# Kernel tuning notes

Measured on AMD Instinct MI355X. Metric: run time of the kernel, lower is better.

Reference implementation:

```python
import jax, jax.numpy as jnp
import numpy as np

B, T, D, H, L, O = 128, 512, 256, 1024, 2, 1


def _cell(x, h, s, Wax, Uas, ba, Wih, Whh, bh):
    # alpha-t gate, exponential smoothing of hidden state, then candidate
    alpha = jax.nn.sigmoid(x @ Wax.T + s @ Uas.T + ba)        # [B,H]
    s_new = alpha * h + (1.0 - alpha) * s                      # smoothed hidden
    h_new = jnp.tanh(x @ Wih.T + s_new @ Whh.T + bh)           # new hidden
    return h_new, s_new


def setup_inputs() -> dict:
    key = jax.random.key(0)
    ks = jax.random.split(key, 12)
    sd_in = 1.0 / np.sqrt(D)
    sd_h = 1.0 / np.sqrt(H)
    return {
        "input": jax.random.normal(ks[0], (B, T, D), dtype=jnp.float32),
        "Wax0": jax.random.normal(ks[1], (H, D), dtype=jnp.float32) * sd_in,
        "Uas0": jax.random.normal(ks[2], (H, H), dtype=jnp.float32) * sd_h,
        "ba0": jnp.zeros((H,), jnp.float32),
        "Wih0": jax.random.normal(ks[3], (H, D), dtype=jnp.float32) * sd_in,
        "Whh0": jax.random.normal(ks[4], (H, H), dtype=jnp.float32) * sd_h,
        "bh0": jnp.zeros((H,), jnp.float32),
        "Wax1": jax.random.normal(ks[5], (H, H), dtype=jnp.float32) * sd_h,
        "Uas1": jax.random.normal(ks[6], (H, H), dtype=jnp.float32) * sd_h,
        "ba1": jnp.zeros((H,), jnp.float32),
        "Wih1": jax.random.normal(ks[7], (H, H), dtype=jnp.float32) * sd_h,
        "Whh1": jax.random.normal(ks[8], (H, H), dtype=jnp.float32) * sd_h,
        "bh1": jnp.zeros((H,), jnp.float32),
        "fc_W": jax.random.normal(ks[9], (O, H), dtype=jnp.float32) * sd_h,
        "fc_b": jnp.zeros((O,), jnp.float32),
    }


def reference(input, Wax0, Uas0, ba0, Wih0, Whh0, bh0,
              Wax1, Uas1, ba1, Wih1, Whh1, bh1, fc_W, fc_b):
    b = input.shape[0]
    zeros = jnp.zeros((b, H), input.dtype)
    carry0 = (zeros, zeros, zeros, zeros)  # h0, s0, h1, s1

    def step(carry, x_t):
        h0, s0, h1, s1 = carry
        h0, s0 = _cell(x_t, h0, s0, Wax0, Uas0, ba0, Wih0, Whh0, bh0)
        h1, s1 = _cell(h0, h1, s1, Wax1, Uas1, ba1, Wih1, Whh1, bh1)
        return (h0, s0, h1, s1), None

    xs = jnp.transpose(input, (1, 0, 2))  # [T,B,D]
    (h0, s0, h1, s1), _ = jax.lax.scan(step, carry0, xs)
    out = h1 @ fc_W.T + fc_b  # [B,O]
    hidden = jnp.stack([h0, h1])          # [L,B,H]
    smoothed = jnp.stack([s0, s1])        # [L,B,H]
    return (out, hidden, smoothed)
```

## Files before the change

kernel.cpp:

```cpp
#include <hip/hip_runtime.h>


typedef unsigned short u16;
typedef unsigned long long u64;
typedef __attribute__((ext_vector_type(8))) short short8;
typedef __attribute__((ext_vector_type(4))) float f32x4;

#define NB   128
#define TT   512
#define DD   256
#define HH   1024
#define NTHR 512
#define SPAN (NB * HH)
#define RING 32
#define GS   16

#define S0_OFF  0u
#define S1_OFF  524288u
#define H0_OFF  1048576u
#define FL_OFF  9437184u
#define W_OFF   9486336u
#define NBIG    6291456u

__device__ __forceinline__ u16 f2bf(float f) {
    unsigned u = __builtin_bit_cast(unsigned, f);
    return (u16)((u + 0x7fffu + ((u >> 16) & 1u)) >> 16);
}
__device__ __forceinline__ u64 agent_load64(const u64* p) {
    return __hip_atomic_load(p, __ATOMIC_RELAXED, __HIP_MEMORY_SCOPE_AGENT);
}
__device__ __forceinline__ void agent_store64(u64* p, u64 v) {
    __hip_atomic_store(p, v, __ATOMIC_RELAXED, __HIP_MEMORY_SCOPE_AGENT);
}

__device__ __forceinline__ void flag_set(unsigned* f, int wgl, unsigned val, int tid)
{
    __syncthreads();
    if (tid == 0)
        __hip_atomic_store(f + wgl * 16, val, __ATOMIC_RELEASE,
                           __HIP_MEMORY_SCOPE_AGENT);
}
__device__ __forceinline__ void flag_wait(unsigned* f, unsigned val, int tid)
{
    if (tid < GS)
        while (__hip_atomic_load(f + tid * 16, __ATOMIC_RELAXED,
                                 __HIP_MEMORY_SCOPE_AGENT) < val)
            __builtin_amdgcn_s_sleep(1);
    __syncthreads();
}

__device__ __forceinline__ void load_frags(short8* fr, const u16* base,
                                           int row, int wv, int lkg)
{
    const u16* sp = base + ((size_t)row << 10) + wv * 128 + lkg * 8;
    #pragma unroll
    for (int s = 0; s < 4; ++s) {
        union { short8 v; u64 q[2]; } u_;
        u_.q[0] = agent_load64((const u64*)(sp + s * 32));
        u_.q[1] = agent_load64((const u64*)(sp + s * 32 + 4));
        fr[s] = u_.v;
    }
}

__device__ __forceinline__ void mm4(f32x4* a, const short8* fr, const u16* W,
                                    int n0, int lrow, int wv, int lkg)
{
    #pragma unroll
    for (int nt = 0; nt < 4; ++nt) {
        const u16* wp = W + ((size_t)(n0 + nt * 16 + lrow) << 10) + wv * 128 + lkg * 8;
        #pragma unroll
        for (int s = 0; s < 4; ++s)
            a[nt] = __builtin_amdgcn_mfma_f32_16x16x32_bf16(
                *(const short8*)(wp + s * 32), fr[s], a[nt], 0, 0, 0);
    }
}

__device__ __forceinline__ void mmx4(f32x4* a, const float* xrow, const u16* W,
                                     int n0, int lrow, int wv, int lkg)
{
    const float* p = xrow + wv * 32 + lkg * 8;
    float4 A = *(const float4*)p;
    float4 B = *(const float4*)(p + 4);
    short8 v;
    v[0]=(short)f2bf(A.x); v[1]=(short)f2bf(A.y); v[2]=(short)f2bf(A.z); v[3]=(short)f2bf(A.w);
    v[4]=(short)f2bf(B.x); v[5]=(short)f2bf(B.y); v[6]=(short)f2bf(B.z); v[7]=(short)f2bf(B.w);
    #pragma unroll
    for (int nt = 0; nt < 4; ++nt) {
        const u16* wp = W + ((size_t)(n0 + nt * 16 + lrow) << 8) + wv * 32 + lkg * 8;
        a[nt] = __builtin_amdgcn_mfma_f32_16x16x32_bf16(
            *(const short8*)wp, v, a[nt], 0, 0, 0);
    }
}

__device__ __forceinline__ void red_put(float (*red)[4][8][64], const f32x4* a,
                                        int wv, int lane)
{
    #pragma unroll
    for (int nt = 0; nt < 4; ++nt)
        #pragma unroll
        for (int c = 0; c < 4; ++c) red[c][nt][wv][lane] = a[nt][c];
}
__device__ __forceinline__ f32x4 red_get(float (*red)[4][8][64], int nt, int lane)
{
    f32x4 v = {0.f, 0.f, 0.f, 0.f};
    #pragma unroll
    for (int j = 0; j < 8; ++j)
        #pragma unroll
        for (int c = 0; c < 4; ++c) v[c] += red[c][nt][j][lane];
    return v;
}

__device__ __forceinline__ u64 pack4(float a, float b, float c, float d)
{
    return (u64)f2bf(a) | ((u64)f2bf(b) << 16) | ((u64)f2bf(c) << 32)
         | ((u64)f2bf(d) << 48);
}

__global__ void conv_weights(const float* Uas0, const float* Whh0, const float* Wax1,
                             const float* Uas1, const float* Wih1, const float* Whh1,
                             const float* Wax0, const float* Wih0, u16* dst)
{
    for (size_t i = (size_t)blockIdx.x * blockDim.x + threadIdx.x; i < 6815744u;
         i += (size_t)gridDim.x * blockDim.x) {
        const float* src; size_t off;
        if (i < NBIG) {
            int seg = (int)(i >> 20); off = i & 1048575u;
            src = seg == 0 ? Uas0 : seg == 1 ? Whh0 : seg == 2 ? Wax1
                : seg == 3 ? Uas1 : seg == 4 ? Wih1 : Whh1;
        } else {
            size_t j = i - NBIG; off = j & 262143u;
            src = (j >> 18) ? Wih0 : Wax0;
        }
        dst[i] = f2bf(src[off]);
    }
}

extern "C" __global__ void __launch_bounds__(NTHR, 1)
alphat_mfma(const float* __restrict__ x,
            const u16* __restrict__ wUas0, const u16* __restrict__ wWhh0,
            const u16* __restrict__ wWax1, const u16* __restrict__ wUas1,
            const u16* __restrict__ wWih1, const u16* __restrict__ wWhh1,
            const u16* __restrict__ wWax0, const u16* __restrict__ wWih0,
            const float* __restrict__ ba0, const float* __restrict__ bh0,
            const float* __restrict__ ba1, const float* __restrict__ bh1,
            const float* __restrict__ fcW, const float* __restrict__ fcb,
            float* __restrict__ out,
            u16* s0b, u16* s1b, u16* h0r, unsigned* flags)
{
    __shared__ float red[4][4][8][64];

    const int tid  = threadIdx.x;
    const int wv   = tid >> 6;
    const int lane = tid & 63;
    const int lrow = lane & 15;
    const int lkg  = lane >> 4;

    const bool isL0 = (blockIdx.x < 128);
    const int wg  = isL0 ? blockIdx.x : (blockIdx.x - 128);
    const int ngg = (wg & 7) * 2 + ((wg >> 3) & 1);
    const int mg  = wg >> 4;
    const int wgl = wg & 15;
    const int m0  = mg * 16;
    const int n0  = ngg * 64;

    unsigned* fB = flags + (size_t)mg * 256;
    unsigned* fC = flags + 2048 + (size_t)mg * 256;
    unsigned* fD = flags + 4096 + (size_t)mg * 256;

    const int arow = m0 + lrow;
    const bool own = (wv < 4);
    const int nb   = n0 + (wv & 3) * 16 + lkg * 4;

    const f32x4 zf = {0.f, 0.f, 0.f, 0.f};
    const size_t HIDB = NB, SMOB = NB + 2 * (size_t)SPAN;

    if (isL0) {
        float4 vba0 = {0,0,0,0}, vbh0 = {0,0,0,0};
        if (own) { vba0 = *(const float4*)(ba0 + nb); vbh0 = *(const float4*)(bh0 + nb); }
        float h0l[4] = {0,0,0,0}, s0l[4] = {0,0,0,0};

        short8 frags[4];
        #pragma unroll
        for (int s = 0; s < 4; ++s)
            #pragma unroll
            for (int i = 0; i < 8; ++i) frags[s][i] = 0;
        const float* xbase = x + (size_t)arow * (TT * DD);
        f32x4 pBx[4], pAx[4];
        #pragma unroll
        for (int nt = 0; nt < 4; ++nt) { pBx[nt] = zf; pAx[nt] = zf; }
        mmx4(pBx, xbase + 0 * DD, wWih0, n0, lrow, wv, lkg);
        mmx4(pAx, xbase + 1 * DD, wWax0, n0, lrow, wv, lkg);

        for (int t = 0; t < TT; ++t) {
            u16* h0cur = h0r + (size_t)(t & (RING - 1)) * SPAN;
            u16* s0nxt = s0b + ((t + 1) & 1) * SPAN;

            if (t >= RING) flag_wait(fC, (unsigned)(t - RING + 1), tid);

            f32x4 acc[4], pA[4];
            #pragma unroll
            for (int nt = 0; nt < 4; ++nt) { acc[nt] = pBx[nt]; pA[nt] = pAx[nt]; }
            mm4(acc, frags, wWhh0, n0, lrow, wv, lkg);
            mm4(pA,  frags, wUas0, n0, lrow, wv, lkg);

            red_put(red, acc, wv, lane);
            __syncthreads();
            f32x4 hsum = zf;
            if (own) hsum = red_get(red, wv, lane);
            __syncthreads();
            red_put(red, pA, wv, lane);
            __syncthreads();
            if (own) {
                f32x4 asum = red_get(red, wv, lane);
                float hb[4];
                #pragma unroll
                for (int r = 0; r < 4; ++r) {
                    hb[r] = tanhf(hsum[r] + ((const float*)&vbh0)[r]);
                    h0l[r] = hb[r];
                }
                agent_store64((u64*)(h0cur + (size_t)(m0 + lrow) * HH + nb),
                              pack4(hb[0], hb[1], hb[2], hb[3]));
                if (t + 1 < TT) {
                    float sb[4];
                    #pragma unroll
                    for (int r = 0; r < 4; ++r) {
                        float al = 1.f / (1.f + __expf(-(asum[r] + ((const float*)&vba0)[r])));
                        sb[r] = al * hb[r] + (1.f - al) * s0l[r];
                        s0l[r] = sb[r];
                    }
                    agent_store64((u64*)(s0nxt + (size_t)(m0 + lrow) * HH + nb),
                                  pack4(sb[0], sb[1], sb[2], sb[3]));
                }
            }
            flag_set(fB, wgl, (unsigned)(t + 1), tid);

            if (t + 1 < TT) {
                #pragma unroll
                for (int nt = 0; nt < 4; ++nt) pBx[nt] = zf;
                mmx4(pBx, xbase + (size_t)(t + 1) * DD, wWih0, n0, lrow, wv, lkg);
                if (t + 2 < TT) {
                    #pragma unroll
                    for (int nt = 0; nt < 4; ++nt) pAx[nt] = zf;
                    mmx4(pAx, xbase + (size_t)(t + 2) * DD, wWax0, n0, lrow, wv, lkg);
                }
                flag_wait(fB, (unsigned)(t + 1), tid);
                load_frags(frags, s0nxt, arow, wv, lkg);
            }
        }
        if (own) {
            const size_t o = (size_t)(m0 + lrow) * HH + nb;
            *(float4*)(out + HIDB + o) = make_float4(h0l[0], h0l[1], h0l[2], h0l[3]);
            *(float4*)(out + SMOB + o) = make_float4(s0l[0], s0l[1], s0l[2], s0l[3]);
        }
    } else {
        float4 vba1 = {0,0,0,0}, vbh1 = {0,0,0,0};
        if (own) { vba1 = *(const float4*)(ba1 + nb); vbh1 = *(const float4*)(bh1 + nb); }
        float h1l[4] = {0,0,0,0}, s1l[4] = {0,0,0,0};
        f32x4 pC1[4];
        #pragma unroll
        for (int nt = 0; nt < 4; ++nt) pC1[nt] = zf;

        for (int t = 0; t < TT; ++t) {
            u16* h0cur = h0r + (size_t)(t & (RING - 1)) * SPAN;
            u16* s1cur = s1b + (t & 1) * SPAN;

            if (t >= 2) flag_wait(fD, (unsigned)(t - 1), tid);

            flag_wait(fB, (unsigned)(t + 1), tid);
            short8 fh[4];
            load_frags(fh, h0cur, arow, wv, lkg);

            f32x4 c[4];
            #pragma unroll
            for (int nt = 0; nt < 4; ++nt) c[nt] = pC1[nt];
            mm4(c, fh, wWax1, n0, lrow, wv, lkg);
            red_put(red, c, wv, lane);
            __syncthreads();
            if (own) {
                f32x4 csum = red_get(red, wv, lane);
                float sb[4];
                #pragma unroll
                for (int r = 0; r < 4; ++r) {
                    float al = 1.f / (1.f + __expf(-(csum[r] + ((const float*)&vba1)[r])));
                    sb[r] = al * h1l[r] + (1.f - al) * s1l[r];
                    s1l[r] = sb[r];
                }
                agent_store64((u64*)(s1cur + (size_t)(m0 + lrow) * HH + nb),
                              pack4(sb[0], sb[1], sb[2], sb[3]));
            }
            flag_set(fC, wgl, (unsigned)(t + 1), tid);

            f32x4 pD1[4];
            #pragma unroll
            for (int nt = 0; nt < 4; ++nt) pD1[nt] = zf;
            mm4(pD1, fh, wWih1, n0, lrow, wv, lkg);

            flag_wait(fC, (unsigned)(t + 1), tid);
            short8 fs1[4];
            load_frags(fs1, s1cur, arow, wv, lkg);
            mm4(pD1, fs1, wWhh1, n0, lrow, wv, lkg);
            #pragma unroll
            for (int nt = 0; nt < 4; ++nt) pC1[nt] = zf;
            mm4(pC1, fs1, wUas1, n0, lrow, wv, lkg);
            red_put(red, pD1, wv, lane);
            __syncthreads();
            if (own) {
                f32x4 dsum = red_get(red, wv, lane);
                #pragma unroll
                for (int r = 0; r < 4; ++r)
                    h1l[r] = tanhf(dsum[r] + ((const float*)&vbh1)[r]);
            }
            flag_set(fD, wgl, (unsigned)(t + 1), tid);
        }
        if (own) {
            const size_t o = (size_t)(m0 + lrow) * HH + nb;
            *(float4*)(out + HIDB + SPAN + o) = make_float4(h1l[0], h1l[1], h1l[2], h1l[3]);
            *(float4*)(out + SMOB + SPAN + o) = make_float4(s1l[0], s1l[1], s1l[2], s1l[3]);

            const float4 w4 = *(const float4*)(fcW + nb);
            float v = h1l[0] * w4.x + h1l[1] * w4.y + h1l[2] * w4.z + h1l[3] * w4.w;
            v += __shfl_xor(v, 16);
            v += __shfl_xor(v, 32);
            if (lane < 16) {
                if (ngg == 0 && wv == 0) v += fcb[0];
                atomicAdd(out + m0 + lane, v);
            }
        }
    }
}

extern "C" void kernel_launch(void* const* d_in, const int* in_sizes, int n_in,
                              void* d_out, int out_size, void* d_ws, size_t ws_size,
                              hipStream_t stream)
{
    const float* x    = (const float*)d_in[0];
    const float* Wax0 = (const float*)d_in[1];
    const float* Uas0 = (const float*)d_in[2];
    const float* ba0  = (const float*)d_in[3];
    const float* Wih0 = (const float*)d_in[4];
    const float* Whh0 = (const float*)d_in[5];
    const float* bh0  = (const float*)d_in[6];
    const float* Wax1 = (const float*)d_in[7];
    const float* Uas1 = (const float*)d_in[8];
    const float* ba1  = (const float*)d_in[9];
    const float* Wih1 = (const float*)d_in[10];
    const float* Whh1 = (const float*)d_in[11];
    const float* bh1  = (const float*)d_in[12];
    const float* fcW  = (const float*)d_in[13];
    const float* fcb  = (const float*)d_in[14];
    float* out = (float*)d_out;

    char* ws = (char*)d_ws;
    u16* s0b = (u16*)(ws + S0_OFF);
    u16* s1b = (u16*)(ws + S1_OFF);
    u16* h0r = (u16*)(ws + H0_OFF);
    unsigned* flags = (unsigned*)(ws + FL_OFF);
    u16* wbase = (u16*)(ws + W_OFF);
    u16* wUas0 = wbase + 0 * 1048576;
    u16* wWhh0 = wbase + 1 * 1048576;
    u16* wWax1 = wbase + 2 * 1048576;
    u16* wUas1 = wbase + 3 * 1048576;
    u16* wWih1 = wbase + 4 * 1048576;
    u16* wWhh1 = wbase + 5 * 1048576;
    u16* wWax0 = wbase + 6 * 1048576;
    u16* wWih0 = wbase + 6 * 1048576 + 262144;

    hipMemsetAsync(d_ws, 0, W_OFF, stream);
    hipMemsetAsync(d_out, 0, (size_t)out_size * sizeof(float), stream);

    conv_weights<<<dim3(1024), dim3(256), 0, stream>>>(
        Uas0, Whh0, Wax1, Uas1, Wih1, Whh1, Wax0, Wih0, wbase);

    alphat_mfma<<<dim3(256), dim3(NTHR), 0, stream>>>(
        x, wUas0, wWhh0, wWax1, wUas1, wWih1, wWhh1, wWax0, wWih0,
        ba0, bh0, ba1, bh1, fcW, fcb, out, s0b, s1b, h0r, flags);
}
```

Baseline: 10.33 ms.

## Replace block-wide flag barriers with per-wave waits and merge reductions

```diff
diff --git a/kernel.cpp b/kernel.cpp
--- a/kernel.cpp
+++ b/kernel.cpp
@@ -35,18 +35,28 @@
 
 __device__ __forceinline__ void flag_set(unsigned* f, int wgl, unsigned val, int tid)
 {
-    __syncthreads();
     if (tid == 0)
         __hip_atomic_store(f + wgl * 16, val, __ATOMIC_RELEASE,
                            __HIP_MEMORY_SCOPE_AGENT);
 }
-__device__ __forceinline__ void flag_wait(unsigned* f, unsigned val, int tid)
-{
-    if (tid < GS)
-        while (__hip_atomic_load(f + tid * 16, __ATOMIC_RELAXED,
+__device__ __forceinline__ void wait2(unsigned* f, int wv, unsigned val, int lane)
+{
+    if (lane < 2) {
+        const int p = lane ? (wv + 8) : wv;
+        while (__hip_atomic_load(f + p * 16, __ATOMIC_RELAXED,
                                  __HIP_MEMORY_SCOPE_AGENT) < val)
             __builtin_amdgcn_s_sleep(1);
-    __syncthreads();
+    }
+    asm volatile("" ::: "memory");
+}
+__device__ __forceinline__ void wait_all(unsigned* f, unsigned val, int lane)
+{
+    if (lane < GS) {
+        while (__hip_atomic_load(f + lane * 16, __ATOMIC_RELAXED,
+                                 __HIP_MEMORY_SCOPE_AGENT) < val)
+            __builtin_amdgcn_s_sleep(1);
+    }
+    asm volatile("" ::: "memory");
 }
 
 __device__ __forceinline__ void load_frags(short8* fr, const u16* base,
@@ -92,22 +102,26 @@
     }
 }
 
-__device__ __forceinline__ void red_put(float (*red)[4][8][64], const f32x4* a,
-                                        int wv, int lane)
+__device__ __forceinline__ void red_put(float (*red)[4][4][7][64], int q,
+                                        const f32x4* a, int wv, int lane)
 {
     #pragma unroll
-    for (int nt = 0; nt < 4; ++nt)
+    for (int nt = 0; nt < 4; ++nt) {
+        if (nt != wv) {
+            const int j = (wv < nt) ? wv : wv - 1;
+            #pragma unroll
+            for (int c = 0; c < 4; ++c) red[q][c][nt][j][lane] = a[nt][c];
+        }
+    }
+}
+__device__ __forceinline__ f32x4 red_get(float (*red)[4][4][7][64], int q,
+                                         f32x4 own, int nt, int lane)
+{
+    #pragma unroll
+    for (int j = 0; j < 7; ++j)
         #pragma unroll
-        for (int c = 0; c < 4; ++c) red[c][nt][wv][lane] = a[nt][c];
-}
-__device__ __forceinline__ f32x4 red_get(float (*red)[4][8][64], int nt, int lane)
-{
-    f32x4 v = {0.f, 0.f, 0.f, 0.f};
-    #pragma unroll
-    for (int j = 0; j < 8; ++j)
-        #pragma unroll
-        for (int c = 0; c < 4; ++c) v[c] += red[c][nt][j][lane];
-    return v;
+        for (int c = 0; c < 4; ++c) own[c] += red[q][c][nt][j][lane];
+    return own;
 }
 
 __device__ __forceinline__ u64 pack4(float a, float b, float c, float d)
@@ -147,7 +161,7 @@
             float* __restrict__ out,
             u16* s0b, u16* s1b, u16* h0r, unsigned* flags)
 {
-    __shared__ float red[4][4][8][64];
+    __shared__ float red[2][4][4][7][64];
 
     const int tid  = threadIdx.x;
     const int wv   = tid >> 6;
@@ -195,7 +209,10 @@
             u16* h0cur = h0r + (size_t)(t & (RING - 1)) * SPAN;
             u16* s0nxt = s0b + ((t + 1) & 1) * SPAN;
 
-            if (t >= RING) flag_wait(fC, (unsigned)(t - RING + 1), tid);
+            if (own) {
+                wait_all(fB, (unsigned)t, lane);
+                if (t >= RING) wait_all(fC, (unsigned)(t - RING + 1), lane);
+            }
 
             f32x4 acc[4], pA[4];
             #pragma unroll
@@ -203,15 +220,16 @@
             mm4(acc, frags, wWhh0, n0, lrow, wv, lkg);
             mm4(pA,  frags, wUas0, n0, lrow, wv, lkg);
 
-            red_put(red, acc, wv, lane);
-            __syncthreads();
-            f32x4 hsum = zf;
-            if (own) hsum = red_get(red, wv, lane);
-            __syncthreads();
-            red_put(red, pA, wv, lane);
+            red_put(red, 0, acc, wv, lane);
+            red_put(red, 1, pA,  wv, lane);
             __syncthreads();
             if (own) {
-                f32x4 asum = red_get(red, wv, lane);
+                f32x4 accOwn = zf, pAOwn = zf;
+                #pragma unroll
+                for (int nt = 0; nt < 4; ++nt)
+                    if (nt == wv) { accOwn = acc[nt]; pAOwn = pA[nt]; }
+                f32x4 hsum = red_get(red, 0, accOwn, wv, lane);
+                f32x4 asum = red_get(red, 1, pAOwn,  wv, lane);
                 float hb[4];
                 #pragma unroll
                 for (int r = 0; r < 4; ++r) {
@@ -232,6 +250,7 @@
                                   pack4(sb[0], sb[1], sb[2], sb[3]));
                 }
             }
+            __syncthreads();
             flag_set(fB, wgl, (unsigned)(t + 1), tid);
 
             if (t + 1 < TT) {
@@ -243,7 +262,7 @@
                     for (int nt = 0; nt < 4; ++nt) pAx[nt] = zf;
                     mmx4(pAx, xbase + (size_t)(t + 2) * DD, wWax0, n0, lrow, wv, lkg);
                 }
-                flag_wait(fB, (unsigned)(t + 1), tid);
+                wait2(fB, wv, (unsigned)(t + 1), lane);
                 load_frags(frags, s0nxt, arow, wv, lkg);
             }
         }
@@ -259,25 +278,34 @@
         f32x4 pC1[4];
         #pragma unroll
         for (int nt = 0; nt < 4; ++nt) pC1[nt] = zf;
+        f32x4 dOwn = zf;
+
+        short8 fh[4];
+        wait2(fB, wv, 1u, lane);
+        load_frags(fh, h0r, arow, wv, lkg);
 
         for (int t = 0; t < TT; ++t) {
-            u16* h0cur = h0r + (size_t)(t & (RING - 1)) * SPAN;
             u16* s1cur = s1b + (t & 1) * SPAN;
 
-            if (t >= 2) flag_wait(fD, (unsigned)(t - 1), tid);
-
-            flag_wait(fB, (unsigned)(t + 1), tid);
-            short8 fh[4];
-            load_frags(fh, h0cur, arow, wv, lkg);
+            if (own && t >= 2) wait_all(fD, (unsigned)(t - 1), lane);
 
             f32x4 c[4];
             #pragma unroll
             for (int nt = 0; nt < 4; ++nt) c[nt] = pC1[nt];
             mm4(c, fh, wWax1, n0, lrow, wv, lkg);
-            red_put(red, c, wv, lane);
+            red_put(red, 0, c, wv, lane);
             __syncthreads();
             if (own) {
-                f32x4 csum = red_get(red, wv, lane);
+                if (t > 0) {
+                    f32x4 dsum = red_get(red, 1, dOwn, wv, lane);
+                    #pragma unroll
+                    for (int r = 0; r < 4; ++r)
+                        h1l[r] = tanhf(dsum[r] + ((const float*)&vbh1)[r]);
+                }
+                f32x4 cOwn = zf;
+                #pragma unroll
+                for (int nt = 0; nt < 4; ++nt) if (nt == wv) cOwn = c[nt];
+                f32x4 csum = red_get(red, 0, cOwn, wv, lane);
                 float sb[4];
                 #pragma unroll
                 for (int r = 0; r < 4; ++r) {
@@ -288,31 +316,39 @@
                 agent_store64((u64*)(s1cur + (size_t)(m0 + lrow) * HH + nb),
                               pack4(sb[0], sb[1], sb[2], sb[3]));
             }
+            __syncthreads();
             flag_set(fC, wgl, (unsigned)(t + 1), tid);
 
             f32x4 pD1[4];
             #pragma unroll
             for (int nt = 0; nt < 4; ++nt) pD1[nt] = zf;
             mm4(pD1, fh, wWih1, n0, lrow, wv, lkg);
-
-            flag_wait(fC, (unsigned)(t + 1), tid);
+            if (t + 1 < TT) {
+                wait2(fB, wv, (unsigned)(t + 2), lane);
+                load_frags(fh, h0r + (size_t)((t + 1) & (RING - 1)) * SPAN,
+                           arow, wv, lkg);
+            }
+
+            wait2(fC, wv, (unsigned)(t + 1), lane);
             short8 fs1[4];
             load_frags(fs1, s1cur, arow, wv, lkg);
             mm4(pD1, fs1, wWhh1, n0, lrow, wv, lkg);
             #pragma unroll
             for (int nt = 0; nt < 4; ++nt) pC1[nt] = zf;
             mm4(pC1, fs1, wUas1, n0, lrow, wv, lkg);
-            red_put(red, pD1, wv, lane);
+            red_put(red, 1, pD1, wv, lane);
+            #pragma unroll
+            for (int nt = 0; nt < 4; ++nt) if (nt == wv) dOwn = pD1[nt];
             __syncthreads();
-            if (own) {
-                f32x4 dsum = red_get(red, wv, lane);
-                #pragma unroll
-                for (int r = 0; r < 4; ++r)
-                    h1l[r] = tanhf(dsum[r] + ((const float*)&vbh1)[r]);
-            }
             flag_set(fD, wgl, (unsigned)(t + 1), tid);
         }
+
         if (own) {
+            f32x4 dsum = red_get(red, 1, dOwn, wv, lane);
+            #pragma unroll
+            for (int r = 0; r < 4; ++r)
+                h1l[r] = tanhf(dsum[r] + ((const float*)&vbh1)[r]);
+
             const size_t o = (size_t)(m0 + lrow) * HH + nb;
             *(float4*)(out + HIDB + SPAN + o) = make_float4(h1l[0], h1l[1], h1l[2], h1l[3]);
             *(float4*)(out + SMOB + SPAN + o) = make_float4(s1l[0], s1l[1], s1l[2], s1l[3]);
```

Measured after the change: 11.80 ms. 14.2% more time.

## Keep recurrent weight tiles in registers and prefetch next-step layer-1 input GEMM

Applied to the files above, without the earlier changes.

```diff
diff --git a/kernel.cpp b/kernel.cpp
--- a/kernel.cpp
+++ b/kernel.cpp
@@ -60,6 +60,27 @@
         u_.q[1] = agent_load64((const u64*)(sp + s * 32 + 4));
         fr[s] = u_.v;
     }
+}
+
+__device__ __forceinline__ void load_wreg(short8* w, const u16* W,
+                                          int n0, int lrow, int wv, int lkg)
+{
+    #pragma unroll
+    for (int nt = 0; nt < 4; ++nt)
+        #pragma unroll
+        for (int s = 0; s < 4; ++s)
+            w[nt * 4 + s] = *(const short8*)(W
+                + ((size_t)(n0 + nt * 16 + lrow) << 10) + wv * 128 + s * 32 + lkg * 8);
+}
+
+__device__ __forceinline__ void mm4r(f32x4* a, const short8* fr, const short8* w)
+{
+    #pragma unroll
+    for (int nt = 0; nt < 4; ++nt)
+        #pragma unroll
+        for (int s = 0; s < 4; ++s)
+            a[nt] = __builtin_amdgcn_mfma_f32_16x16x32_bf16(
+                w[nt * 4 + s], fr[s], a[nt], 0, 0, 0);
 }
 
 __device__ __forceinline__ void mm4(f32x4* a, const short8* fr, const u16* W,
@@ -175,6 +196,10 @@
     const size_t HIDB = NB, SMOB = NB + 2 * (size_t)SPAN;
 
     if (isL0) {
+        short8 wh[16], wu[16];
+        load_wreg(wh, wWhh0, n0, lrow, wv, lkg);
+        load_wreg(wu, wUas0, n0, lrow, wv, lkg);
+
         float4 vba0 = {0,0,0,0}, vbh0 = {0,0,0,0};
         if (own) { vba0 = *(const float4*)(ba0 + nb); vbh0 = *(const float4*)(bh0 + nb); }
         float h0l[4] = {0,0,0,0}, s0l[4] = {0,0,0,0};
@@ -200,8 +225,8 @@
             f32x4 acc[4], pA[4];
             #pragma unroll
             for (int nt = 0; nt < 4; ++nt) { acc[nt] = pBx[nt]; pA[nt] = pAx[nt]; }
-            mm4(acc, frags, wWhh0, n0, lrow, wv, lkg);
-            mm4(pA,  frags, wUas0, n0, lrow, wv, lkg);
+            mm4r(acc, frags, wh);
+            mm4r(pA,  frags, wu);
 
             red_put(red, acc, wv, lane);
             __syncthreads();
@@ -253,27 +278,32 @@
             *(float4*)(out + SMOB + o) = make_float4(s0l[0], s0l[1], s0l[2], s0l[3]);
         }
     } else {
+        short8 wu1[16], wh1[16];
+        load_wreg(wu1, wUas1, n0, lrow, wv, lkg);
+        load_wreg(wh1, wWhh1, n0, lrow, wv, lkg);
+
         float4 vba1 = {0,0,0,0}, vbh1 = {0,0,0,0};
         if (own) { vba1 = *(const float4*)(ba1 + nb); vbh1 = *(const float4*)(bh1 + nb); }
         float h1l[4] = {0,0,0,0}, s1l[4] = {0,0,0,0};
-        f32x4 pC1[4];
+        f32x4 pC1[4], cAx[4];
         #pragma unroll
         for (int nt = 0; nt < 4; ++nt) pC1[nt] = zf;
 
+        short8 fh[4];
+        flag_wait(fB, 1u, tid);
+        load_frags(fh, h0r, arow, wv, lkg);
+        #pragma unroll
+        for (int nt = 0; nt < 4; ++nt) cAx[nt] = zf;
+        mm4(cAx, fh, wWax1, n0, lrow, wv, lkg);
+
         for (int t = 0; t < TT; ++t) {
-            u16* h0cur = h0r + (size_t)(t & (RING - 1)) * SPAN;
             u16* s1cur = s1b + (t & 1) * SPAN;
 
             if (t >= 2) flag_wait(fD, (unsigned)(t - 1), tid);
-
-            flag_wait(fB, (unsigned)(t + 1), tid);
-            short8 fh[4];
-            load_frags(fh, h0cur, arow, wv, lkg);
 
             f32x4 c[4];
             #pragma unroll
-            for (int nt = 0; nt < 4; ++nt) c[nt] = pC1[nt];
-            mm4(c, fh, wWax1, n0, lrow, wv, lkg);
+            for (int nt = 0; nt < 4; ++nt) c[nt] = pC1[nt] + cAx[nt];
             red_put(red, c, wv, lane);
             __syncthreads();
             if (own) {
@@ -294,14 +324,22 @@
             #pragma unroll
             for (int nt = 0; nt < 4; ++nt) pD1[nt] = zf;
             mm4(pD1, fh, wWih1, n0, lrow, wv, lkg);
+            if (t + 1 < TT) {
+                flag_wait(fB, (unsigned)(t + 2), tid);
+                load_frags(fh, h0r + (size_t)((t + 1) & (RING - 1)) * SPAN,
+                           arow, wv, lkg);
+                #pragma unroll
+                for (int nt = 0; nt < 4; ++nt) cAx[nt] = zf;
+                mm4(cAx, fh, wWax1, n0, lrow, wv, lkg);
+            }
 
             flag_wait(fC, (unsigned)(t + 1), tid);
             short8 fs1[4];
             load_frags(fs1, s1cur, arow, wv, lkg);
-            mm4(pD1, fs1, wWhh1, n0, lrow, wv, lkg);
+            mm4r(pD1, fs1, wh1);
             #pragma unroll
             for (int nt = 0; nt < 4; ++nt) pC1[nt] = zf;
-            mm4(pC1, fs1, wUas1, n0, lrow, wv, lkg);
+            mm4r(pC1, fs1, wu1);
             red_put(red, pD1, wv, lane);
             __syncthreads();
             if (own) {
```

Result: slower. 11.62 ms (+12.5%).
